# Optimization experiments

Measured on AMD Instinct MI355X. Metric: run time of the kernel, lower is better.

## Reference

```python
import jax, jax.numpy as jnp
import numpy as np

B, T, D, U = 32, 4096, 512, 256

def setup_inputs() -> dict:
    key = jax.random.key(0)
    ks = jax.random.split(key, 5)
    s = 1.0 / np.sqrt(D)
    return {
        "values": jax.random.normal(ks[0], (B, T, D), dtype=jnp.float32),
        "query": jax.random.normal(ks[1], (B, D), dtype=jnp.float32),
        "W1": jax.random.normal(ks[2], (D, U), dtype=jnp.float32) * s,
        "b1": jnp.zeros((U,), dtype=jnp.float32),
        "W2": jax.random.normal(ks[3], (D, U), dtype=jnp.float32) * s,
        "b2": jnp.zeros((U,), dtype=jnp.float32),
        "V": jax.random.normal(ks[4], (U, 1), dtype=jnp.float32) * (1.0 / np.sqrt(U)),
        "bV": jnp.zeros((1,), dtype=jnp.float32),
    }

def reference(values, query, W1, b1, W2, b2, V, bV):
    # values: [B,T,D], query: [B,D]
    h_vals = jnp.einsum('btd,du->btu', values, W1) + b1          # [B,T,U]
    h_query = (query @ W2 + b2)[:, None, :]                       # [B,1,U]
    score = jnp.einsum('btu,uo->bto', jnp.tanh(h_vals + h_query), V) + bV  # [B,T,1]
    attention_weights = jax.nn.softmax(score, axis=1)             # [B,T,1]
    context_vector = jnp.sum(attention_weights * values, axis=1)  # [B,D]
    return context_vector, attention_weights
```

## Files before the change

### kernel.cpp

```cpp
#include <hip/hip_runtime.h>
#include <math.h>
#include <stdint.h>

#define BB 32
#define TT 4096
#define DD 512
#define UU 256

#define KC 32
#define NKC (DD/KC)
#define LDB 40
#define TC 256

typedef __attribute__((ext_vector_type(8))) short short8;
typedef __attribute__((ext_vector_type(8))) unsigned short ushort8;
typedef __attribute__((ext_vector_type(4))) float floatx4;

__device__ __forceinline__ unsigned short bf16_rne(float x) {
  union { float f; uint32_t u; } v; v.f = x;
  uint32_t r = v.u + 0x7FFFu + ((v.u >> 16) & 1u);
  return (unsigned short)(r >> 16);
}
__device__ __forceinline__ float tanh_fast(float x) {
  float e = __expf(2.0f * x);
  return 1.0f - 2.0f * __builtin_amdgcn_rcpf(e + 1.0f);
}

__global__ __launch_bounds__(256) void prep_w1_kernel(
    const float* __restrict__ W1, unsigned short* __restrict__ staged) {
  const int kc = blockIdx.x;
  const int u = threadIdx.x;
  __attribute__((aligned(16))) unsigned short row[LDB];
#pragma unroll
  for (int kk = 0; kk < KC; ++kk)
    row[kk] = bf16_rne(W1[(kc * KC + kk) * UU + u]);
#pragma unroll
  for (int kk = KC; kk < LDB; ++kk) row[kk] = 0;
  unsigned short* dst = staged + ((size_t)kc * UU + u) * LDB;
#pragma unroll
  for (int i = 0; i < 5; ++i) ((uint4*)dst)[i] = *(const uint4*)&row[i * 8];
}

__global__ __launch_bounds__(256) void hquery_kernel(
    const float* __restrict__ query, const float* __restrict__ W2,
    const float* __restrict__ b2, const float* __restrict__ b1,
    float* __restrict__ hq) {
  const int b = blockIdx.x;
  const int u = threadIdx.x;
  __shared__ float q[DD];
  for (int d = threadIdx.x; d < DD; d += 256) q[d] = query[b * DD + d];
  __syncthreads();
  float acc = b2[u] + b1[u];
  for (int d = 0; d < DD; ++d) acc += q[d] * W2[d * UU + u];
  hq[b * UU + u] = acc;
}

__global__ __launch_bounds__(256) void score_kernel(
    const float* __restrict__ values, const unsigned short* __restrict__ w1s,
    const float* __restrict__ hq, const float* __restrict__ V,
    const float* __restrict__ bV, float* __restrict__ scores) {
  const int b = blockIdx.y;
  const int t0 = blockIdx.x * 64;
  const int tid = threadIdx.x;
  const int wave = tid >> 6;
  const int lane = tid & 63;
  const int c = lane & 15;
  const int q = lane >> 4;

  __shared__ unsigned short As[64 * LDB];
  __shared__ unsigned short Bs[UU * LDB];
  __shared__ float red[64][17];

  for (int i = tid; i < 64 * 17; i += 256) ((float*)red)[i] = 0.0f;

  floatx4 acc[4][4];
#pragma unroll
  for (int ti = 0; ti < 4; ++ti)
#pragma unroll
    for (int ui = 0; ui < 4; ++ui) acc[ti][ui] = (floatx4){0.f, 0.f, 0.f, 0.f};

  const size_t vbase = ((size_t)b * TT + t0) * DD;
  const int ar = tid >> 2;
  const int aseg = tid & 3;

  for (int kc = 0; kc < NKC; ++kc) {
    __syncthreads();
    {
      const float* src = values + vbase + (size_t)ar * DD + kc * KC + aseg * 8;
      const float4 f0 = *(const float4*)src;
      const float4 f1 = *(const float4*)(src + 4);
      ushort8 t8;
      t8[0] = bf16_rne(f0.x); t8[1] = bf16_rne(f0.y);
      t8[2] = bf16_rne(f0.z); t8[3] = bf16_rne(f0.w);
      t8[4] = bf16_rne(f1.x); t8[5] = bf16_rne(f1.y);
      t8[6] = bf16_rne(f1.z); t8[7] = bf16_rne(f1.w);
      *(ushort8*)&As[ar * LDB + aseg * 8] = t8;
    }
    {
      const uint4* src = (const uint4*)(w1s + (size_t)kc * UU * LDB);
      uint4* dst = (uint4*)Bs;
#pragma unroll
      for (int i = 0; i < 5; ++i) dst[i * 256 + tid] = src[i * 256 + tid];
    }
    __syncthreads();
    short8 afr[4], bfr[4];
#pragma unroll
    for (int ti = 0; ti < 4; ++ti)
      afr[ti] = *(const short8*)&As[(ti * 16 + c) * LDB + q * 8];
#pragma unroll
    for (int ui = 0; ui < 4; ++ui)
      bfr[ui] = *(const short8*)&Bs[(wave * 64 + ui * 16 + c) * LDB + q * 8];
#pragma unroll
    for (int ti = 0; ti < 4; ++ti)
#pragma unroll
      for (int ui = 0; ui < 4; ++ui)
        acc[ti][ui] = __builtin_amdgcn_mfma_f32_16x16x32_bf16(
            afr[ti], bfr[ui], acc[ti][ui], 0, 0, 0);
  }

  float hqv[4], vv[4];
#pragma unroll
  for (int ui = 0; ui < 4; ++ui) {
    const int u = wave * 64 + ui * 16 + c;
    hqv[ui] = hq[b * UU + u];
    vv[ui] = V[u];
  }
#pragma unroll
  for (int ti = 0; ti < 4; ++ti)
#pragma unroll
    for (int r = 0; r < 4; ++r) {
      const int t = ti * 16 + q * 4 + r;
      float e = 0.0f;
#pragma unroll
      for (int ui = 0; ui < 4; ++ui)
        e += tanh_fast(acc[ti][ui][r] + hqv[ui]) * vv[ui];
      atomicAdd(&red[t][c], e);
    }
  __syncthreads();
  if (tid < 64) {
    float s = bV[0];
#pragma unroll
    for (int x = 0; x < 16; ++x) s += red[tid][x];
    scores[b * TT + t0 + tid] = s;
  }
}

__global__ __launch_bounds__(256) void softmax_stats_kernel(
    const float* __restrict__ scores, float* __restrict__ stats) {
  const int b = blockIdx.x;
  const int tid = threadIdx.x;
  __shared__ float sm[256];
  float m = -1e30f;
  for (int t = tid; t < TT; t += 256) m = fmaxf(m, scores[b * TT + t]);
  sm[tid] = m;
  __syncthreads();
  for (int s = 128; s > 0; s >>= 1) {
    if (tid < s) sm[tid] = fmaxf(sm[tid], sm[tid + s]);
    __syncthreads();
  }
  m = sm[0];
  __syncthreads();
  float l = 0.0f;
  for (int t = tid; t < TT; t += 256) l += __expf(scores[b * TT + t] - m);
  sm[tid] = l;
  __syncthreads();
  for (int s = 128; s > 0; s >>= 1) {
    if (tid < s) sm[tid] += sm[tid + s];
    __syncthreads();
  }
  if (tid == 0) {
    stats[2 * b] = m;
    stats[2 * b + 1] = sm[0];
  }
}

__global__ __launch_bounds__(256) void context_kernel(
    const float* __restrict__ values, const float* __restrict__ scores,
    const float* __restrict__ stats, float* __restrict__ out) {
  const int b = blockIdx.y;
  const int tc0 = blockIdx.x * TC;
  const int tid = threadIdx.x;
  const float m = stats[2 * b];
  const float linv = 1.0f / stats[2 * b + 1];

  __shared__ float wts[TC];
  {
    const float w = __expf(scores[b * TT + tc0 + tid] - m) * linv;
    wts[tid] = w;
    out[BB * DD + b * TT + tc0 + tid] = w;
  }
  __syncthreads();

  const int sub = tid >> 7;
  const int d4 = tid & 127;
  const float4* vp = (const float4*)(values + ((size_t)b * TT + tc0) * DD);
  float4 acc = {0.f, 0.f, 0.f, 0.f};
#pragma unroll 4
  for (int t = sub; t < TC; t += 2) {
    const float w = wts[t];
    const float4 v = vp[(size_t)t * (DD / 4) + d4];
    acc.x += w * v.x; acc.y += w * v.y; acc.z += w * v.z; acc.w += w * v.w;
  }
  float* o = out + b * DD + d4 * 4;
  atomicAdd(o + 0, acc.x);
  atomicAdd(o + 1, acc.y);
  atomicAdd(o + 2, acc.z);
  atomicAdd(o + 3, acc.w);
}

extern "C" void kernel_launch(void* const* d_in, const int* in_sizes, int n_in,
                              void* d_out, int out_size, void* d_ws, size_t ws_size,
                              hipStream_t stream) {
  const float* values = (const float*)d_in[0];
  const float* query  = (const float*)d_in[1];
  const float* W1     = (const float*)d_in[2];
  const float* b1     = (const float*)d_in[3];
  const float* W2     = (const float*)d_in[4];
  const float* b2     = (const float*)d_in[5];
  const float* V      = (const float*)d_in[6];
  const float* bV     = (const float*)d_in[7];
  float* out = (float*)d_out;

  float* ws = (float*)d_ws;
  float* hq     = ws;
  float* scores = ws + BB * UU;
  float* stats  = scores + BB * TT;
  unsigned short* w1s = (unsigned short*)(stats + 2 * BB);

  hipMemsetAsync(out, 0, BB * DD * sizeof(float), stream);

  prep_w1_kernel<<<NKC, 256, 0, stream>>>(W1, w1s);
  hquery_kernel<<<BB, 256, 0, stream>>>(query, W2, b2, b1, hq);
  score_kernel<<<dim3(TT / 64, BB), 256, 0, stream>>>(values, w1s, hq, V, bV, scores);
  softmax_stats_kernel<<<BB, 256, 0, stream>>>(scores, stats);
  context_kernel<<<dim3(TT / TC, BB), 256, 0, stream>>>(values, scores, stats, out);
}
```

Measured before the change: 487.0 us.

## Prefetch values tile into registers, use direct-to-LDS W1 loads, shuffle reduction

In the score kernel, the next K-chunk of values is loaded into registers while the current chunk's MFMAs run, which hides global load latency. The W1 tile copy now uses global_load_lds, so it goes straight from global memory to LDS without passing through VGPRs. The per-row score reduction replaces LDS atomics with wave shuffles and a small per-wave buffer. The prefetch costs extra registers and adds a dependency on how global_load_lds is synchronized.

Result: faster. 464.0 us (-4.7%).

```diff
diff --git a/kernel.cpp b/kernel.cpp
--- a/kernel.cpp
+++ b/kernel.cpp
@@ -15,6 +15,9 @@
 typedef __attribute__((ext_vector_type(8))) short short8;
 typedef __attribute__((ext_vector_type(8))) unsigned short ushort8;
 typedef __attribute__((ext_vector_type(4))) float floatx4;
+
+typedef const __attribute__((address_space(1))) unsigned int GU32;
+typedef __attribute__((address_space(3))) unsigned int LU32;
 
 __device__ __forceinline__ unsigned short bf16_rne(float x) {
   union { float f; uint32_t u; } v; v.f = x;
@@ -47,11 +50,11 @@
     float* __restrict__ hq) {
   const int b = blockIdx.x;
   const int u = threadIdx.x;
-  __shared__ float q[DD];
-  for (int d = threadIdx.x; d < DD; d += 256) q[d] = query[b * DD + d];
+  __shared__ float qs[DD];
+  for (int d = threadIdx.x; d < DD; d += 256) qs[d] = query[b * DD + d];
   __syncthreads();
   float acc = b2[u] + b1[u];
-  for (int d = 0; d < DD; ++d) acc += q[d] * W2[d * UU + u];
+  for (int d = 0; d < DD; ++d) acc += qs[d] * W2[d * UU + u];
   hq[b * UU + u] = acc;
 }
 
@@ -69,9 +72,7 @@
 
   __shared__ unsigned short As[64 * LDB];
   __shared__ unsigned short Bs[UU * LDB];
-  __shared__ float red[64][17];
-
-  for (int i = tid; i < 64 * 17; i += 256) ((float*)red)[i] = 0.0f;
+  __shared__ float redW[4][64];
 
   floatx4 acc[4][4];
 #pragma unroll
@@ -79,30 +80,34 @@
 #pragma unroll
     for (int ui = 0; ui < 4; ++ui) acc[ti][ui] = (floatx4){0.f, 0.f, 0.f, 0.f};
 
-  const size_t vbase = ((size_t)b * TT + t0) * DD;
   const int ar = tid >> 2;
   const int aseg = tid & 3;
+  const float* asrc =
+      values + ((size_t)b * TT + t0) * DD + (size_t)ar * DD + aseg * 8;
+
+  float4 a0 = *(const float4*)asrc;
+  float4 a1 = *(const float4*)(asrc + 4);
 
   for (int kc = 0; kc < NKC; ++kc) {
     __syncthreads();
     {
-      const float* src = values + vbase + (size_t)ar * DD + kc * KC + aseg * 8;
-      const float4 f0 = *(const float4*)src;
-      const float4 f1 = *(const float4*)(src + 4);
       ushort8 t8;
-      t8[0] = bf16_rne(f0.x); t8[1] = bf16_rne(f0.y);
-      t8[2] = bf16_rne(f0.z); t8[3] = bf16_rne(f0.w);
-      t8[4] = bf16_rne(f1.x); t8[5] = bf16_rne(f1.y);
-      t8[6] = bf16_rne(f1.z); t8[7] = bf16_rne(f1.w);
+      t8[0] = bf16_rne(a0.x); t8[1] = bf16_rne(a0.y);
+      t8[2] = bf16_rne(a0.z); t8[3] = bf16_rne(a0.w);
+      t8[4] = bf16_rne(a1.x); t8[5] = bf16_rne(a1.y);
+      t8[6] = bf16_rne(a1.z); t8[7] = bf16_rne(a1.w);
       *(ushort8*)&As[ar * LDB + aseg * 8] = t8;
     }
     {
-      const uint4* src = (const uint4*)(w1s + (size_t)kc * UU * LDB);
-      uint4* dst = (uint4*)Bs;
-#pragma unroll
-      for (int i = 0; i < 5; ++i) dst[i * 256 + tid] = src[i * 256 + tid];
-    }
-    __syncthreads();
+      GU32* src = (GU32*)(w1s + (size_t)kc * UU * LDB);
+      LU32* dst = (LU32*)Bs;
+#pragma unroll
+      for (int i = 0; i < 5; ++i)
+        __builtin_amdgcn_global_load_lds(src + (i * 256 + tid) * 4,
+                                         dst + (i * 256 + tid) * 4, 16, 0, 0);
+    }
+    __syncthreads();
+
     short8 afr[4], bfr[4];
 #pragma unroll
     for (int ti = 0; ti < 4; ++ti)
@@ -116,6 +121,11 @@
       for (int ui = 0; ui < 4; ++ui)
         acc[ti][ui] = __builtin_amdgcn_mfma_f32_16x16x32_bf16(
             afr[ti], bfr[ui], acc[ti][ui], 0, 0, 0);
+
+    if (kc + 1 < NKC) {
+      a0 = *(const float4*)(asrc + (kc + 1) * KC);
+      a1 = *(const float4*)(asrc + (kc + 1) * KC + 4);
+    }
   }
 
   float hqv[4], vv[4];
@@ -129,18 +139,20 @@
   for (int ti = 0; ti < 4; ++ti)
 #pragma unroll
     for (int r = 0; r < 4; ++r) {
-      const int t = ti * 16 + q * 4 + r;
       float e = 0.0f;
 #pragma unroll
       for (int ui = 0; ui < 4; ++ui)
         e += tanh_fast(acc[ti][ui][r] + hqv[ui]) * vv[ui];
-      atomicAdd(&red[t][c], e);
+      e += __shfl_xor(e, 1, 64);
+      e += __shfl_xor(e, 2, 64);
+      e += __shfl_xor(e, 4, 64);
+      e += __shfl_xor(e, 8, 64);
+      if (c == 0) redW[wave][ti * 16 + q * 4 + r] = e;
     }
   __syncthreads();
   if (tid < 64) {
-    float s = bV[0];
-#pragma unroll
-    for (int x = 0; x < 16; ++x) s += red[tid][x];
+    const float s =
+        bV[0] + redW[0][tid] + redW[1][tid] + redW[2][tid] + redW[3][tid];
     scores[b * TT + t0 + tid] = s;
   }
 }
```
